# Kernel tuning notes

Measured on AMD Instinct MI355X. Metric: run time of the kernel, lower is better.

Reference implementation:

```python
import jax, jax.numpy as jnp
import numpy as np

B, T, D = 4, 4096, 1024

def setup_inputs() -> dict:
    key = jax.random.key(0)
    ks = jax.random.split(key, 6)
    x = jax.random.normal(ks[0], (B, T, D), dtype=jnp.float32)
    mask = jax.random.randint(ks[1], (B, T), 0, 2).astype(bool)
    # torch nn.Linear init scale ~ 1/sqrt(fan_in); exact init unimportant for correctness baseline
    s = 1.0 / np.sqrt(D)
    W_qkv = jax.random.normal(ks[2], (3 * D, D), dtype=jnp.float32) * s
    b_qkv = jax.random.normal(ks[3], (3 * D,), dtype=jnp.float32) * s
    W_out = jax.random.normal(ks[4], (D, D), dtype=jnp.float32) * s
    b_out = jax.random.normal(ks[5], (D,), dtype=jnp.float32) * s
    return {"x": x, "mask": mask, "W_qkv": W_qkv, "b_qkv": b_qkv, "W_out": W_out, "b_out": b_out}

def reference(x, mask, W_qkv, b_qkv, W_out, b_out):
    # qkv projection: (B,T,D) @ (D,3D) + (3D,)
    qkv = jnp.einsum('btd,ed->bte', x, W_qkv) + b_qkv
    q, k, v = jnp.split(qkv, 3, axis=-1)  # each (B,T,D)
    q = q / jnp.linalg.norm(q, axis=-1, keepdims=True)
    k = k / jnp.linalg.norm(k, axis=-1, keepdims=True)
    k = jnp.where(mask[..., None], 0.0, k)  # masked_fill(mask, 0)
    kv = jnp.sum(k * v, axis=-2, keepdims=True)  # (B,1,D) global feature sum
    out = kv * q  # (B,T,D)
    return jnp.einsum('btd,ed->bte', out, W_out) + b_out
```

## Files before the change

kernel.cpp:

```cpp
#include <hip/hip_runtime.h>
#include <stdint.h>


typedef short  short8  __attribute__((ext_vector_type(8)));
typedef float  floatx4 __attribute__((ext_vector_type(4)));

#define BM 128
#define BN 128
#define BK 32

__device__ __forceinline__ void async16(const void* g, void* l) {
  __builtin_amdgcn_global_load_lds((const __attribute__((address_space(1))) void*)g,
                                   (__attribute__((address_space(3))) void*)l, 16, 0, 0);
}

__device__ __forceinline__ uint16_t f2bf(float f) {
  union { float f; uint32_t u; } x; x.f = f;
  uint32_t u = x.u;
  return (uint16_t)((u + 0x7fffu + ((u >> 16) & 1u)) >> 16);
}
__device__ __forceinline__ float bf2f(uint16_t h) {
  union { uint32_t u; float f; } x; x.u = ((uint32_t)h) << 16; return x.f;
}
__device__ __forceinline__ uint32_t pack2(float a, float b) {
  return (uint32_t)f2bf(a) | ((uint32_t)f2bf(b) << 16);
}
__device__ __forceinline__ void upk8(uint4 u, float* f) {
  f[0]=bf2f((uint16_t)u.x); f[1]=bf2f((uint16_t)(u.x>>16));
  f[2]=bf2f((uint16_t)u.y); f[3]=bf2f((uint16_t)(u.y>>16));
  f[4]=bf2f((uint16_t)u.z); f[5]=bf2f((uint16_t)(u.z>>16));
  f[6]=bf2f((uint16_t)u.w); f[7]=bf2f((uint16_t)(u.w>>16));
}

__global__ __launch_bounds__(256) void cvt_bf16(const float* __restrict__ in,
                                                uint16_t* __restrict__ out, int n8) {
  int i = blockIdx.x * blockDim.x + threadIdx.x;
  if (i >= n8) return;
  const float4* p = (const float4*)in;
  float4 a = p[(size_t)i * 2], b = p[(size_t)i * 2 + 1];
  uint4 o;
  o.x = pack2(a.x, a.y); o.y = pack2(a.z, a.w);
  o.z = pack2(b.x, b.y); o.w = pack2(b.z, b.w);
  ((uint4*)out)[i] = o;
}

template <int WRITE_BF16>
__global__ __launch_bounds__(256, 2) void gemm_bt(
    const uint16_t* __restrict__ A, const uint16_t* __restrict__ Bw,
    const float* __restrict__ bias, float* __restrict__ Cf,
    uint16_t* __restrict__ Cb, int M, int N, int K)
{
  __shared__ __align__(16) uint16_t As[BM * BK];
  __shared__ __align__(16) uint16_t Bs[BN * BK];
  const int tid  = threadIdx.x;
  const int wave = tid >> 6, lane = tid & 63;
  const int quad = lane >> 4, r16 = lane & 15;
  const int wm = wave & 1, wn = wave >> 1;
  const int tileM = blockIdx.y * BM, tileN = blockIdx.x * BN;

  const int c0 = wave * 64 + lane, c1 = c0 + 256;
  const size_t ga0 = (size_t)(tileM + (c0 >> 2)) * K + (c0 & 3) * 8;
  const size_t ga1 = (size_t)(tileM + (c1 >> 2)) * K + (c1 & 3) * 8;
  const size_t gb0 = (size_t)(tileN + (c0 >> 2)) * K + (c0 & 3) * 8;
  const size_t gb1 = (size_t)(tileN + (c1 >> 2)) * K + (c1 & 3) * 8;
  char* lA0 = (char*)As + (wave * 64) * 16;
  char* lA1 = (char*)As + (256 + wave * 64) * 16;
  char* lB0 = (char*)Bs + (wave * 64) * 16;
  char* lB1 = (char*)Bs + (256 + wave * 64) * 16;

  floatx4 acc[4][4];
#pragma unroll
  for (int i = 0; i < 4; i++)
#pragma unroll
    for (int j = 0; j < 4; j++) acc[i][j] = (floatx4){0.f, 0.f, 0.f, 0.f};

  for (int k0 = 0; k0 < K; k0 += BK) {
    async16(A + ga0 + k0, lA0);
    async16(A + ga1 + k0, lA1);
    async16(Bw + gb0 + k0, lB0);
    async16(Bw + gb1 + k0, lB1);
    __syncthreads();

    short8 af[4], bf[4];
#pragma unroll
    for (int mi = 0; mi < 4; mi++)
      af[mi] = *(const short8*)&As[(wm * 64 + mi * 16 + r16) * BK + quad * 8];
#pragma unroll
    for (int ni = 0; ni < 4; ni++)
      bf[ni] = *(const short8*)&Bs[(wn * 64 + ni * 16 + r16) * BK + quad * 8];
#pragma unroll
    for (int mi = 0; mi < 4; mi++)
#pragma unroll
      for (int ni = 0; ni < 4; ni++)
        acc[mi][ni] = __builtin_amdgcn_mfma_f32_16x16x32_bf16(af[mi], bf[ni], acc[mi][ni], 0, 0, 0);
    __syncthreads();
  }

#pragma unroll
  for (int mi = 0; mi < 4; mi++) {
    int rg = tileM + wm * 64 + mi * 16 + quad * 4;
#pragma unroll
    for (int ni = 0; ni < 4; ni++) {
      int cg = tileN + wn * 64 + ni * 16 + r16;
      float bv = bias[cg];
#pragma unroll
      for (int i = 0; i < 4; i++) {
        float v = acc[mi][ni][i] + bv;
        if (WRITE_BF16) Cb[(size_t)(rg + i) * N + cg] = f2bf(v);
        else            Cf[(size_t)(rg + i) * N + cg] = v;
      }
    }
  }
}

__global__ __launch_bounds__(256) void detect_mask(const unsigned char* __restrict__ m,
                                                   int* __restrict__ flag) {
  int i = blockIdx.x * blockDim.x + threadIdx.x;
  int v = ((i & 3) != 0) ? (int)m[i] : 0;
  unsigned long long b = __ballot(v != 0);
  if ((threadIdx.x & 63) == 0 && b) atomicOr(flag, 1);
}

__global__ __launch_bounds__(256) void rownorm_kv(
    const uint16_t* __restrict__ qkv, const void* __restrict__ maskbuf,
    const int* __restrict__ flag, float* __restrict__ invq, float* __restrict__ kv)
{
  __shared__ float kvloc[1024];
  const int tid = threadIdx.x;
  for (int i = tid; i < 1024; i += 256) kvloc[i] = 0.f;
  __syncthreads();
  const int wave = tid >> 6, lane = tid & 63;
  const int b = blockIdx.x >> 7;
  const int chunk = blockIdx.x & 127;
  const int isU8 = *flag;
  const unsigned char* m8 = (const unsigned char*)maskbuf;
  const int* m32 = (const int*)maskbuf;

  float kvacc[16];
#pragma unroll
  for (int i = 0; i < 16; i++) kvacc[i] = 0.f;

  const int r0 = b * 4096 + chunk * 32 + wave * 8;
  for (int j = 0; j < 8; j++) {
    int r = r0 + j;
    const uint16_t* rp = qkv + (size_t)r * 3072;
    uint4 q0 = *(const uint4*)(rp + lane * 16);
    uint4 q1 = *(const uint4*)(rp + lane * 16 + 8);
    uint4 k0 = *(const uint4*)(rp + 1024 + lane * 16);
    uint4 k1 = *(const uint4*)(rp + 1024 + lane * 16 + 8);
    uint4 v0 = *(const uint4*)(rp + 2048 + lane * 16);
    uint4 v1 = *(const uint4*)(rp + 2048 + lane * 16 + 8);
    float qf[16], kf[16], vf[16];
    upk8(q0, qf); upk8(q1, qf + 8);
    upk8(k0, kf); upk8(k1, kf + 8);
    upk8(v0, vf); upk8(v1, vf + 8);
    float sq = 0.f, sk = 0.f;
#pragma unroll
    for (int i = 0; i < 16; i++) { sq = fmaf(qf[i], qf[i], sq); sk = fmaf(kf[i], kf[i], sk); }
    for (int off = 32; off; off >>= 1) { sq += __shfl_xor(sq, off); sk += __shfl_xor(sk, off); }
    float rq = rsqrtf(sq), rk = rsqrtf(sk);
    if (lane == 0) invq[r] = rq;
    int masked = isU8 ? (int)m8[r] : m32[r];
    if (!masked) {
#pragma unroll
      for (int i = 0; i < 16; i++) kvacc[i] = fmaf(kf[i] * rk, vf[i], kvacc[i]);
    }
  }
#pragma unroll
  for (int i = 0; i < 16; i++) atomicAdd(&kvloc[lane * 16 + i], kvacc[i]);
  __syncthreads();
  for (int i = tid; i < 1024; i += 256) atomicAdd(&kv[b * 1024 + i], kvloc[i]);
}

__global__ __launch_bounds__(256) void scale_q(
    const uint16_t* __restrict__ qkv, const float* __restrict__ invq,
    const float* __restrict__ kv, uint16_t* __restrict__ outb)
{
  int i = blockIdx.x * blockDim.x + threadIdx.x;
  int e = i << 3;
  int r = e >> 10;
  int d = e & 1023;
  int b = r >> 12;
  float s = invq[r];
  uint4 qv = *(const uint4*)(qkv + (size_t)r * 3072 + d);
  const float* kp = kv + (b << 10) + d;
  float qf[8]; upk8(qv, qf);
  uint4 o;
  o.x = pack2(qf[0] * s * kp[0], qf[1] * s * kp[1]);
  o.y = pack2(qf[2] * s * kp[2], qf[3] * s * kp[3]);
  o.z = pack2(qf[4] * s * kp[4], qf[5] * s * kp[5]);
  o.w = pack2(qf[6] * s * kp[6], qf[7] * s * kp[7]);
  *(uint4*)(outb + (size_t)r * 1024 + d) = o;
}

extern "C" void kernel_launch(void* const* d_in, const int* in_sizes, int n_in,
                              void* d_out, int out_size, void* d_ws, size_t ws_size,
                              hipStream_t stream) {
  const float* x     = (const float*)d_in[0];
  const void*  mask  = d_in[1];
  const float* W_qkv = (const float*)d_in[2];
  const float* b_qkv = (const float*)d_in[3];
  const float* W_out = (const float*)d_in[4];
  const float* b_out = (const float*)d_in[5];
  float* out = (float*)d_out;

  const int BT = 4 * 4096;
  const int D  = 1024;

  char* ws = (char*)d_ws;
  size_t off = 0;
  auto alloc = [&](size_t bytes) { size_t r = off; off += (bytes + 255) & ~(size_t)255; return r; };
  size_t o_xb   = alloc((size_t)BT * D * 2);
  size_t o_qkvb = alloc((size_t)BT * 3 * D * 2);
  size_t o_wq   = alloc((size_t)3 * D * D * 2);
  size_t o_wo   = alloc((size_t)D * D * 2);
  size_t o_kv   = alloc((size_t)4 * D * 4 + 256);
  size_t o_invq = alloc((size_t)BT * 4);

  uint16_t* xb   = (uint16_t*)(ws + o_xb);
  uint16_t* qkvb = (uint16_t*)(ws + o_qkvb);
  uint16_t* wq   = (uint16_t*)(ws + o_wq);
  uint16_t* wo   = (uint16_t*)(ws + o_wo);
  float*    kv   = (float*)(ws + o_kv);
  int*      flag = (int*)(ws + o_kv + (size_t)4 * D * 4);
  float*    invq = (float*)(ws + o_invq);
  uint16_t* outb = xb;

  hipMemsetAsync(ws + o_kv, 0, (size_t)4 * D * 4 + 256, stream);
  cvt_bf16<<<dim3(BT * D / 8 / 256), 256, 0, stream>>>(x, xb, BT * D / 8);
  cvt_bf16<<<dim3(3 * D * D / 8 / 256), 256, 0, stream>>>(W_qkv, wq, 3 * D * D / 8);
  cvt_bf16<<<dim3(D * D / 8 / 256), 256, 0, stream>>>(W_out, wo, D * D / 8);
  gemm_bt<1><<<dim3(3 * D / BN, BT / BM), 256, 0, stream>>>(xb, wq, b_qkv, nullptr, qkvb, BT, 3 * D, D);
  detect_mask<<<dim3(64), 256, 0, stream>>>((const unsigned char*)mask, flag);
  rownorm_kv<<<dim3(512), 256, 0, stream>>>(qkvb, mask, flag, invq, kv);
  scale_q<<<dim3(BT * D / 8 / 256), 256, 0, stream>>>(qkvb, invq, kv, outb);
  gemm_bt<0><<<dim3(D / BN, BT / BM), 256, 0, stream>>>(outb, wo, b_out, out, nullptr, BT, D, D);
}
```

Measured before the change: 349.7 us.

## Switch GEMMs to 32x32x16 MFMA with BK=64 swizzled LDS, fuse scale into out-GEMM

Result: faster. 342.2 us (-2.2%).

```diff
diff --git a/kernel.cpp b/kernel.cpp
--- a/kernel.cpp
+++ b/kernel.cpp
@@ -2,12 +2,12 @@
 #include <stdint.h>
 
 
-typedef short  short8  __attribute__((ext_vector_type(8)));
-typedef float  floatx4 __attribute__((ext_vector_type(4)));
+typedef short  short8   __attribute__((ext_vector_type(8)));
+typedef float  floatx16 __attribute__((ext_vector_type(16)));
 
 #define BM 128
 #define BN 128
-#define BK 32
+#define BK 64
 
 __device__ __forceinline__ void async16(const void* g, void* l) {
   __builtin_amdgcn_global_load_lds((const __attribute__((address_space(1))) void*)g,
@@ -32,82 +32,193 @@
   f[6]=bf2f((uint16_t)u.w); f[7]=bf2f((uint16_t)(u.w>>16));
 }
 
-__global__ __launch_bounds__(256) void cvt_bf16(const float* __restrict__ in,
-                                                uint16_t* __restrict__ out, int n8) {
-  int i = blockIdx.x * blockDim.x + threadIdx.x;
-  if (i >= n8) return;
+__global__ __launch_bounds__(256) void cvt3(
+    const float* __restrict__ a, uint16_t* __restrict__ ao, int na,
+    const float* __restrict__ b, uint16_t* __restrict__ bo, int nb,
+    const float* __restrict__ c, uint16_t* __restrict__ co, int nc) {
+  int i = blockIdx.x * 256 + threadIdx.x;
+  const float* in; uint16_t* out; int j = i;
+  if (j < na) { in = a; out = ao; }
+  else {
+    j -= na;
+    if (j < nb) { in = b; out = bo; }
+    else { j -= nb; if (j >= nc) return; in = c; out = co; }
+  }
   const float4* p = (const float4*)in;
-  float4 a = p[(size_t)i * 2], b = p[(size_t)i * 2 + 1];
+  float4 u = p[(size_t)j * 2], v = p[(size_t)j * 2 + 1];
   uint4 o;
-  o.x = pack2(a.x, a.y); o.y = pack2(a.z, a.w);
-  o.z = pack2(b.x, b.y); o.w = pack2(b.z, b.w);
-  ((uint4*)out)[i] = o;
-}
-
-template <int WRITE_BF16>
-__global__ __launch_bounds__(256, 2) void gemm_bt(
+  o.x = pack2(u.x, u.y); o.y = pack2(u.z, u.w);
+  o.z = pack2(v.x, v.y); o.w = pack2(v.z, v.w);
+  ((uint4*)out)[j] = o;
+}
+
+__global__ __launch_bounds__(256, 2) void gemm1(
     const uint16_t* __restrict__ A, const uint16_t* __restrict__ Bw,
-    const float* __restrict__ bias, float* __restrict__ Cf,
-    uint16_t* __restrict__ Cb, int M, int N, int K)
+    const float* __restrict__ bias, uint16_t* __restrict__ Cb,
+    int N, int K)
 {
   __shared__ __align__(16) uint16_t As[BM * BK];
   __shared__ __align__(16) uint16_t Bs[BN * BK];
-  const int tid  = threadIdx.x;
+  const int tid = threadIdx.x;
   const int wave = tid >> 6, lane = tid & 63;
-  const int quad = lane >> 4, r16 = lane & 15;
+  const int l31 = lane & 31, khalf = lane >> 5;
   const int wm = wave & 1, wn = wave >> 1;
   const int tileM = blockIdx.y * BM, tileN = blockIdx.x * BN;
 
-  const int c0 = wave * 64 + lane, c1 = c0 + 256;
-  const size_t ga0 = (size_t)(tileM + (c0 >> 2)) * K + (c0 & 3) * 8;
-  const size_t ga1 = (size_t)(tileM + (c1 >> 2)) * K + (c1 & 3) * 8;
-  const size_t gb0 = (size_t)(tileN + (c0 >> 2)) * K + (c0 & 3) * 8;
-  const size_t gb1 = (size_t)(tileN + (c1 >> 2)) * K + (c1 & 3) * 8;
-  char* lA0 = (char*)As + (wave * 64) * 16;
-  char* lA1 = (char*)As + (256 + wave * 64) * 16;
-  char* lB0 = (char*)Bs + (wave * 64) * 16;
-  char* lB1 = (char*)Bs + (256 + wave * 64) * 16;
-
-  floatx4 acc[4][4];
-#pragma unroll
-  for (int i = 0; i < 4; i++)
-#pragma unroll
-    for (int j = 0; j < 4; j++) acc[i][j] = (floatx4){0.f, 0.f, 0.f, 0.f};
+  const int srow = wave * 8 + (lane >> 3);
+  const int skc  = (lane & 7) ^ (lane >> 3);
+  const uint16_t* gA = A  + (size_t)(tileM + srow) * K + skc * 8;
+  const uint16_t* gB = Bw + (size_t)(tileN + srow) * K + skc * 8;
+  char* lA = (char*)As + wave * 64 * 16;
+  char* lB = (char*)Bs + wave * 64 * 16;
+
+  floatx16 acc[2][2];
+#pragma unroll
+  for (int mi = 0; mi < 2; mi++)
+#pragma unroll
+    for (int ni = 0; ni < 2; ni++)
+#pragma unroll
+      for (int r = 0; r < 16; r++) acc[mi][ni][r] = 0.f;
+
+  const int arow0 = wm * 64 + l31;
+  const int brow0 = wn * 64 + l31;
 
   for (int k0 = 0; k0 < K; k0 += BK) {
-    async16(A + ga0 + k0, lA0);
-    async16(A + ga1 + k0, lA1);
-    async16(Bw + gb0 + k0, lB0);
-    async16(Bw + gb1 + k0, lB1);
+#pragma unroll
+    for (int s = 0; s < 4; s++) {
+      async16(gA + k0 + s * 32 * K, lA + s * 4096);
+      async16(gB + k0 + s * 32 * K, lB + s * 4096);
+    }
     __syncthreads();
-
-    short8 af[4], bf[4];
-#pragma unroll
-    for (int mi = 0; mi < 4; mi++)
-      af[mi] = *(const short8*)&As[(wm * 64 + mi * 16 + r16) * BK + quad * 8];
-#pragma unroll
-    for (int ni = 0; ni < 4; ni++)
-      bf[ni] = *(const short8*)&Bs[(wn * 64 + ni * 16 + r16) * BK + quad * 8];
-#pragma unroll
-    for (int mi = 0; mi < 4; mi++)
-#pragma unroll
-      for (int ni = 0; ni < 4; ni++)
-        acc[mi][ni] = __builtin_amdgcn_mfma_f32_16x16x32_bf16(af[mi], bf[ni], acc[mi][ni], 0, 0, 0);
+#pragma unroll
+    for (int ks = 0; ks < 4; ks++) {
+      const int kc = khalf + ks * 2;
+      short8 af[2], bfr[2];
+#pragma unroll
+      for (int mi = 0; mi < 2; mi++) {
+        int r = arow0 + mi * 32;
+        af[mi] = *(const short8*)&As[(r * 8 + (kc ^ (r & 7))) * 8];
+      }
+#pragma unroll
+      for (int ni = 0; ni < 2; ni++) {
+        int r = brow0 + ni * 32;
+        bfr[ni] = *(const short8*)&Bs[(r * 8 + (kc ^ (r & 7))) * 8];
+      }
+#pragma unroll
+      for (int mi = 0; mi < 2; mi++)
+#pragma unroll
+        for (int ni = 0; ni < 2; ni++)
+          acc[mi][ni] = __builtin_amdgcn_mfma_f32_32x32x16_bf16(af[mi], bfr[ni], acc[mi][ni], 0, 0, 0);
+    }
     __syncthreads();
   }
 
 #pragma unroll
-  for (int mi = 0; mi < 4; mi++) {
-    int rg = tileM + wm * 64 + mi * 16 + quad * 4;
-#pragma unroll
-    for (int ni = 0; ni < 4; ni++) {
-      int cg = tileN + wn * 64 + ni * 16 + r16;
-      float bv = bias[cg];
-#pragma unroll
-      for (int i = 0; i < 4; i++) {
-        float v = acc[mi][ni][i] + bv;
-        if (WRITE_BF16) Cb[(size_t)(rg + i) * N + cg] = f2bf(v);
-        else            Cf[(size_t)(rg + i) * N + cg] = v;
+  for (int mi = 0; mi < 2; mi++) {
+    int rbase = tileM + wm * 64 + mi * 32 + 4 * khalf;
+#pragma unroll
+    for (int ni = 0; ni < 2; ni++) {
+      int col = tileN + wn * 64 + ni * 32 + l31;
+      float bv = bias[col];
+#pragma unroll
+      for (int reg = 0; reg < 16; reg++) {
+        int row = rbase + (reg & 3) + 8 * (reg >> 2);
+        Cb[(size_t)row * N + col] = f2bf(acc[mi][ni][reg] + bv);
+      }
+    }
+  }
+}
+
+__global__ __launch_bounds__(256, 2) void gemm2(
+    const uint16_t* __restrict__ qkv, const float* __restrict__ invq,
+    const float* __restrict__ kv, const uint16_t* __restrict__ Bw,
+    const float* __restrict__ bias, float* __restrict__ Cf,
+    int N, int K)
+{
+  __shared__ __align__(16) uint16_t As[BM * BK];
+  __shared__ __align__(16) uint16_t Bs[BN * BK];
+  const int tid = threadIdx.x;
+  const int wave = tid >> 6, lane = tid & 63;
+  const int l31 = lane & 31, khalf = lane >> 5;
+  const int wm = wave & 1, wn = wave >> 1;
+  const int tileM = blockIdx.y * BM, tileN = blockIdx.x * BN;
+
+  const int srow = wave * 8 + (lane >> 3);
+  const int skc  = (lane & 7) ^ (lane >> 3);
+  const uint16_t* gB = Bw + (size_t)(tileN + srow) * K + skc * 8;
+  char* lB = (char*)Bs + wave * 64 * 16;
+  const float* kvb = kv + ((tileM >> 12) << 10);
+
+  float sinv[4];
+#pragma unroll
+  for (int s = 0; s < 4; s++) sinv[s] = invq[tileM + s * 32 + srow];
+
+  floatx16 acc[2][2];
+#pragma unroll
+  for (int mi = 0; mi < 2; mi++)
+#pragma unroll
+    for (int ni = 0; ni < 2; ni++)
+#pragma unroll
+      for (int r = 0; r < 16; r++) acc[mi][ni][r] = 0.f;
+
+  const int arow0 = wm * 64 + l31;
+  const int brow0 = wn * 64 + l31;
+
+  for (int k0 = 0; k0 < K; k0 += BK) {
+#pragma unroll
+    for (int s = 0; s < 4; s++)
+      async16(gB + k0 + s * 32 * K, lB + s * 4096);
+#pragma unroll
+    for (int s = 0; s < 4; s++) {
+      int r = tileM + s * 32 + srow;
+      int d = k0 + skc * 8;
+      uint4 qv = *(const uint4*)(qkv + (size_t)r * 3072 + d);
+      float4 k0v = *(const float4*)(kvb + d);
+      float4 k1v = *(const float4*)(kvb + d + 4);
+      float qf[8]; upk8(qv, qf);
+      float sc = sinv[s];
+      uint4 o;
+      o.x = pack2(qf[0] * sc * k0v.x, qf[1] * sc * k0v.y);
+      o.y = pack2(qf[2] * sc * k0v.z, qf[3] * sc * k0v.w);
+      o.z = pack2(qf[4] * sc * k1v.x, qf[5] * sc * k1v.y);
+      o.w = pack2(qf[6] * sc * k1v.z, qf[7] * sc * k1v.w);
+      *(uint4*)((char*)As + (size_t)(s * 256 + wave * 64 + lane) * 16) = o;
+    }
+    __syncthreads();
+#pragma unroll
+    for (int ks = 0; ks < 4; ks++) {
+      const int kc = khalf + ks * 2;
+      short8 af[2], bfr[2];
+#pragma unroll
+      for (int mi = 0; mi < 2; mi++) {
+        int r = arow0 + mi * 32;
+        af[mi] = *(const short8*)&As[(r * 8 + (kc ^ (r & 7))) * 8];
+      }
+#pragma unroll
+      for (int ni = 0; ni < 2; ni++) {
+        int r = brow0 + ni * 32;
+        bfr[ni] = *(const short8*)&Bs[(r * 8 + (kc ^ (r & 7))) * 8];
+      }
+#pragma unroll
+      for (int mi = 0; mi < 2; mi++)
+#pragma unroll
+        for (int ni = 0; ni < 2; ni++)
+          acc[mi][ni] = __builtin_amdgcn_mfma_f32_32x32x16_bf16(af[mi], bfr[ni], acc[mi][ni], 0, 0, 0);
+    }
+    __syncthreads();
+  }
+
+#pragma unroll
+  for (int mi = 0; mi < 2; mi++) {
+    int rbase = tileM + wm * 64 + mi * 32 + 4 * khalf;
+#pragma unroll
+    for (int ni = 0; ni < 2; ni++) {
+      int col = tileN + wn * 64 + ni * 32 + l31;
+      float bv = bias[col];
+#pragma unroll
+      for (int reg = 0; reg < 16; reg++) {
+        int row = rbase + (reg & 3) + 8 * (reg >> 2);
+        Cf[(size_t)row * N + col] = acc[mi][ni][reg] + bv;
       }
     }
   }
@@ -172,27 +283,6 @@
   for (int i = tid; i < 1024; i += 256) atomicAdd(&kv[b * 1024 + i], kvloc[i]);
 }
 
-__global__ __launch_bounds__(256) void scale_q(
-    const uint16_t* __restrict__ qkv, const float* __restrict__ invq,
-    const float* __restrict__ kv, uint16_t* __restrict__ outb)
-{
-  int i = blockIdx.x * blockDim.x + threadIdx.x;
-  int e = i << 3;
-  int r = e >> 10;
-  int d = e & 1023;
-  int b = r >> 12;
-  float s = invq[r];
-  uint4 qv = *(const uint4*)(qkv + (size_t)r * 3072 + d);
-  const float* kp = kv + (b << 10) + d;
-  float qf[8]; upk8(qv, qf);
-  uint4 o;
-  o.x = pack2(qf[0] * s * kp[0], qf[1] * s * kp[1]);
-  o.y = pack2(qf[2] * s * kp[2], qf[3] * s * kp[3]);
-  o.z = pack2(qf[4] * s * kp[4], qf[5] * s * kp[5]);
-  o.w = pack2(qf[6] * s * kp[6], qf[7] * s * kp[7]);
-  *(uint4*)(outb + (size_t)r * 1024 + d) = o;
-}
-
 extern "C" void kernel_launch(void* const* d_in, const int* in_sizes, int n_in,
                               void* d_out, int out_size, void* d_ws, size_t ws_size,
                               hipStream_t stream) {
@@ -224,15 +314,15 @@
   float*    kv   = (float*)(ws + o_kv);
   int*      flag = (int*)(ws + o_kv + (size_t)4 * D * 4);
   float*    invq = (float*)(ws + o_invq);
-  uint16_t* outb = xb;
 
   hipMemsetAsync(ws + o_kv, 0, (size_t)4 * D * 4 + 256, stream);
-  cvt_bf16<<<dim3(BT * D / 8 / 256), 256, 0, stream>>>(x, xb, BT * D / 8);
-  cvt_bf16<<<dim3(3 * D * D / 8 / 256), 256, 0, stream>>>(W_qkv, wq, 3 * D * D / 8);
-  cvt_bf16<<<dim3(D * D / 8 / 256), 256, 0, stream>>>(W_out, wo, D * D / 8);
-  gemm_bt<1><<<dim3(3 * D / BN, BT / BM), 256, 0, stream>>>(xb, wq, b_qkv, nullptr, qkvb, BT, 3 * D, D);
+  {
+    int na = BT * D / 8, nb = 3 * D * D / 8, nc = D * D / 8;
+    int tot = na + nb + nc;
+    cvt3<<<dim3((tot + 255) / 256), 256, 0, stream>>>(x, xb, na, W_qkv, wq, nb, W_out, wo, nc);
+  }
   detect_mask<<<dim3(64), 256, 0, stream>>>((const unsigned char*)mask, flag);
+  gemm1<<<dim3(3 * D / BN, BT / BM), 256, 0, stream>>>(xb, wq, b_qkv, qkvb, 3 * D, D);
   rownorm_kv<<<dim3(512), 256, 0, stream>>>(qkvb, mask, flag, invq, kv);
-  scale_q<<<dim3(BT * D / 8 / 256), 256, 0, stream>>>(qkvb, invq, kv, outb);
-  gemm_bt<0><<<dim3(D / BN, BT / BM), 256, 0, stream>>>(outb, wo, b_out, out, nullptr, BT, D, D);
-}
+  gemm2<<<dim3(D / BN, BT / BM), 256, 0, stream>>>(qkvb, invq, kv, wo, b_out, out, D, D);
+}
```
